# Kernel tuning notes

Measured on AMD Instinct MI355X. Metric: run time of the kernel, lower is better.

The kernel has to match this reference:

```python
import jax, jax.numpy as jnp
import numpy as np

MAX_SENT_LEN = 28
B, LAT, D, E = 2048, 256, 1024, 256
LN_EPS = 1e-5


def setup_inputs() -> dict:
    key = jax.random.key(0)
    ks = jax.random.split(key, 10)
    s = 0.05
    return {
        "z": jax.random.normal(ks[0], (B, LAT), jnp.float32),
        "true_inp": jax.random.normal(ks[1], (B, MAX_SENT_LEN, E), jnp.float32),
        "tf_mask": jax.random.bernoulli(ks[2], 0.5, (MAX_SENT_LEN,)),
        "fc_w": jax.random.normal(ks[3], (D, LAT), jnp.float32) * s,
        "fc_b": jnp.zeros((D,), jnp.float32),
        "ln_w": jnp.ones((D,), jnp.float32),
        "ln_b": jnp.zeros((D,), jnp.float32),
        "w_ih": jax.random.normal(ks[4], (3 * D, D), jnp.float32) * s,
        "b_ih": jnp.zeros((3 * D,), jnp.float32),
        "w_hh": jax.random.normal(ks[5], (3 * D, D), jnp.float32) * s,
        "b_hh": jnp.zeros((3 * D,), jnp.float32),
    }


def reference(z, true_inp, tf_mask, fc_w, fc_b, ln_w, ln_b, w_ih, b_ih, w_hh, b_hh):
    # fc + layer norm -> initial hidden and (repeated) step input, [B, D]
    x = z @ fc_w.T + fc_b
    mu = jnp.mean(x, axis=-1, keepdims=True)
    var = jnp.mean(jnp.square(x - mu), axis=-1, keepdims=True)
    x = (x - mu) * jax.lax.rsqrt(var + LN_EPS) * ln_w + ln_b

    # encoded input is identical at every step -> precompute input gates once
    gi = x @ w_ih.T + b_ih                      # [B, 3D]
    i_r, i_z, i_n = jnp.split(gi, 3, axis=-1)

    # true_inp.repeat(1,1,repeating).transpose(1,0) -> [T, B, D]
    rep = D // E
    true_rep = jnp.transpose(jnp.tile(true_inp, (1, 1, rep)), (1, 0, 2))

    def step(h, inputs):
        t_inp, m = inputs
        h_in = jnp.where(m, t_inp, h)           # teacher-forcing branch
        gh = h_in @ w_hh.T + b_hh               # [B, 3D]
        h_r, h_z, h_n = jnp.split(gh, 3, axis=-1)
        r = jax.nn.sigmoid(i_r + h_r)
        u = jax.nn.sigmoid(i_z + h_z)
        n = jnp.tanh(i_n + r * h_n)
        h_new = (1.0 - u) * n + u * h_in
        return h_new, h_new

    _, outs = jax.lax.scan(step, x, (true_rep, tf_mask))
    return outs                                  # [T, B, D]
```

## Files before the change

### kernel.cpp

```cpp
#include <hip/hip_runtime.h>
#include <hip/hip_bf16.h>

#define TSTEPS 28

typedef __attribute__((ext_vector_type(8))) short bf16x8;
typedef __attribute__((ext_vector_type(4))) float f32x4;
typedef __attribute__((ext_vector_type(4))) unsigned short u16x4;
typedef __hip_bfloat16 bf16;

__device__ __forceinline__ unsigned short f2b(float f) {
  bf16 h = __float2bfloat16(f);
  return *reinterpret_cast<unsigned short*>(&h);
}
__device__ __forceinline__ float b2f(unsigned short u) {
  bf16 h = *reinterpret_cast<bf16*>(&u);
  return __bfloat162float(h);
}

__device__ __forceinline__ void gload16(const void* g, void* l) {
  __builtin_amdgcn_global_load_lds(
      (const __attribute__((address_space(1))) void*)g,
      (__attribute__((address_space(3))) void*)l, 16, 0, 0);
}

__device__ __forceinline__ float sigm(float x) { return 1.f / (1.f + __expf(-x)); }
__device__ __forceinline__ float tanh_fast(float x) {
  const float e2 = __expf(2.f * x);
  return 1.f - 2.f / (e2 + 1.f);
}

__device__ __forceinline__ bf16x8 cvt8(const float* src) {
  const float4 v0 = *(const float4*)src;
  const float4 v1 = *(const float4*)(src + 4);
  bf16x8 sv;
  sv[0] = (short)f2b(v0.x); sv[1] = (short)f2b(v0.y);
  sv[2] = (short)f2b(v0.z); sv[3] = (short)f2b(v0.w);
  sv[4] = (short)f2b(v1.x); sv[5] = (short)f2b(v1.y);
  sv[6] = (short)f2b(v1.z); sv[7] = (short)f2b(v1.w);
  return sv;
}

__global__ void conv_kernel(const float* __restrict__ in, unsigned short* __restrict__ out, int n4) {
  int i = blockIdx.x * blockDim.x + threadIdx.x;
  const int stride = gridDim.x * blockDim.x;
  for (; i < n4; i += stride) {
    const float4 v = *(const float4*)&in[(size_t)i * 4];
    u16x4 o;
    o.x = f2b(v.x); o.y = f2b(v.y); o.z = f2b(v.z); o.w = f2b(v.w);
    *(u16x4*)&out[(size_t)i * 4] = o;
  }
}

__global__ __launch_bounds__(256) void convw_kernel(const float* __restrict__ whh,
                                                    unsigned short* __restrict__ whhb,
                                                    unsigned short* __restrict__ whf) {
  const int idx = blockIdx.x * 256 + threadIdx.x;
  const int n = idx >> 6, k4 = (idx & 63) << 2;
  const float* r = &whh[(size_t)n * 1024 + k4];
  const float4 a = *(const float4*)r;
  const float4 b = *(const float4*)(r + 256);
  const float4 c = *(const float4*)(r + 512);
  const float4 d = *(const float4*)(r + 768);
  u16x4 oa, ob, oc, od, of;
  oa.x = f2b(a.x); oa.y = f2b(a.y); oa.z = f2b(a.z); oa.w = f2b(a.w);
  ob.x = f2b(b.x); ob.y = f2b(b.y); ob.z = f2b(b.z); ob.w = f2b(b.w);
  oc.x = f2b(c.x); oc.y = f2b(c.y); oc.z = f2b(c.z); oc.w = f2b(c.w);
  od.x = f2b(d.x); od.y = f2b(d.y); od.z = f2b(d.z); od.w = f2b(d.w);
  of.x = f2b(a.x + b.x + c.x + d.x);
  of.y = f2b(a.y + b.y + c.y + d.y);
  of.z = f2b(a.z + b.z + c.z + d.z);
  of.w = f2b(a.w + b.w + c.w + d.w);
  unsigned short* wb = &whhb[(size_t)n * 1024 + k4];
  *(u16x4*)(wb)       = oa;
  *(u16x4*)(wb + 256) = ob;
  *(u16x4*)(wb + 512) = oc;
  *(u16x4*)(wb + 768) = od;
  *(u16x4*)&whf[(size_t)n * 256 + k4] = of;
}

__global__ __launch_bounds__(256, 2) void gemm_fc_kernel(
    const float* __restrict__ A, const float* __restrict__ W,
    const float* __restrict__ bias, float* __restrict__ out) {
  constexpr int K = 256, NT = K / 32;
  __shared__ __align__(16) bf16 lds[2][6144];
  const int tid = threadIdx.x;
  const int lane = tid & 63;
  const int l15 = lane & 15, l4 = lane >> 4;
  const int wid = tid >> 6, wm = wid >> 1, wn = wid & 1;
  const int m0 = blockIdx.x * 128, n0 = blockIdx.y * 64;
  const int ra = tid >> 2, cb = (tid & 3) * 8;

  f32x4 acc[4][2] = {};

  auto STAGE = [&](int buf, int kt) {
    const int k0 = kt * 32;
    *(bf16x8*)&lds[buf][tid * 8]        = cvt8(&A[(size_t)(m0 + ra) * K + k0 + cb]);
    *(bf16x8*)&lds[buf][2048 + tid * 8] = cvt8(&A[(size_t)(m0 + 64 + ra) * K + k0 + cb]);
    *(bf16x8*)&lds[buf][4096 + tid * 8] = cvt8(&W[(size_t)(n0 + ra) * K + k0 + cb]);
  };

  STAGE(0, 0);
  __syncthreads();
  for (int kt = 0; kt < NT; ++kt) {
    const int buf = kt & 1;
    if (kt + 1 < NT) STAGE(buf ^ 1, kt + 1);
    bf16x8 af[4], bfr[2];
#pragma unroll
    for (int m = 0; m < 4; ++m)
      af[m] = *(const bf16x8*)&lds[buf][(wm * 64 + m * 16 + l15) * 32 + l4 * 8];
#pragma unroll
    for (int n = 0; n < 2; ++n)
      bfr[n] = *(const bf16x8*)&lds[buf][4096 + (wn * 32 + n * 16 + l15) * 32 + l4 * 8];
#pragma unroll
    for (int m = 0; m < 4; ++m)
#pragma unroll
      for (int n = 0; n < 2; ++n)
        acc[m][n] = __builtin_amdgcn_mfma_f32_16x16x32_bf16(af[m], bfr[n], acc[m][n], 0, 0, 0);
    __syncthreads();
  }

#pragma unroll
  for (int m = 0; m < 4; ++m) {
#pragma unroll
    for (int n = 0; n < 2; ++n) {
      const int col = n0 + wn * 32 + n * 16 + l15;
      const int rowb = m0 + wm * 64 + m * 16 + l4 * 4;
      const float bv = bias[col];
#pragma unroll
      for (int r = 0; r < 4; ++r)
        out[(size_t)(rowb + r) * 1024 + col] = acc[m][n][r] + bv;
    }
  }
}

__global__ __launch_bounds__(256) void ln_kernel(const float* __restrict__ x,
                                                 const float* __restrict__ w,
                                                 const float* __restrict__ b,
                                                 bf16* __restrict__ h0b,
                                                 float* __restrict__ h0f) {
  const int row = blockIdx.x, tid = threadIdx.x;
  const float4 v = *(const float4*)&x[(size_t)row * 1024 + tid * 4];
  float vv[4] = {v.x, v.y, v.z, v.w};
  float s = vv[0] + vv[1] + vv[2] + vv[3];
  float sq = vv[0] * vv[0] + vv[1] * vv[1] + vv[2] * vv[2] + vv[3] * vv[3];
#pragma unroll
  for (int off = 32; off; off >>= 1) {
    s += __shfl_down(s, off);
    sq += __shfl_down(sq, off);
  }
  __shared__ float sa[4], sb[4];
  const int lane = tid & 63, wid = tid >> 6;
  if (lane == 0) { sa[wid] = s; sb[wid] = sq; }
  __syncthreads();
  s = sa[0] + sa[1] + sa[2] + sa[3];
  sq = sb[0] + sb[1] + sb[2] + sb[3];
  const float mu = s * (1.f / 1024.f);
  const float var = sq * (1.f / 1024.f) - mu * mu;
  const float rs = rsqrtf(var + 1e-5f);
#pragma unroll
  for (int j = 0; j < 4; ++j) {
    const int c = tid * 4 + j;
    const float xv = (vv[j] - mu) * rs * w[c] + b[c];
    h0b[(size_t)row * 1024 + c] = __float2bfloat16(xv);
    h0f[(size_t)row * 1024 + c] = xv;
  }
}

__global__ __launch_bounds__(512, 4) void gemm_gi_kernel(
    const bf16* __restrict__ A,
    const float* __restrict__ W,
    const float* __restrict__ bias,
    unsigned short* __restrict__ out) {
  __shared__ __align__(16) bf16 lds[2][16384];
  const int tid = threadIdx.x;
  const int lane = tid & 63, l15 = lane & 15, l4 = lane >> 4;
  const int wid = tid >> 6, wm = wid >> 2, wn = wid & 3;
  const int n0 = blockIdx.x * 64, m0 = blockIdx.y * 64;

  f32x4 acc[3][2] = {};

  auto STAGE = [&](int buf, int kt) {
    const int k0 = kt * 64;
    {
      const int c = tid;
      const int row = c >> 3, kk = ((c & 7) ^ (row & 7)) * 8;
      gload16(&A[(size_t)(m0 + row) * 1024 + k0 + kk], &lds[buf][c * 8]);
    }
#pragma unroll
    for (int j = 0; j < 3; ++j) {
      const int c = tid + j * 512;
      const int row = c >> 3, kk = ((c & 7) ^ (row & 7)) * 8;
      *(bf16x8*)&lds[buf][4096 + c * 8] =
          cvt8(&W[(size_t)((row >> 6) * 1024 + n0 + (row & 63)) * 1024 + k0 + kk]);
    }
  };

  STAGE(0, 0);
  __syncthreads();
  for (int kt = 0; kt < 16; ++kt) {
    const int buf = kt & 1;
    if (kt + 1 < 16) STAGE(buf ^ 1, kt + 1);
#pragma unroll
    for (int ks = 0; ks < 2; ++ks) {
      const int x = (((ks << 2) | l4) ^ (l15 & 7)) * 8;
      bf16x8 af[2], bfr[3];
#pragma unroll
      for (int m = 0; m < 2; ++m)
        af[m] = *(const bf16x8*)&lds[buf][(wm * 32 + m * 16 + l15) * 64 + x];
#pragma unroll
      for (int g = 0; g < 3; ++g)
        bfr[g] = *(const bf16x8*)&lds[buf][4096 + (g * 64 + wn * 16 + l15) * 64 + x];
#pragma unroll
      for (int g = 0; g < 3; ++g)
#pragma unroll
        for (int m = 0; m < 2; ++m)
          acc[g][m] = __builtin_amdgcn_mfma_f32_16x16x32_bf16(af[m], bfr[g], acc[g][m], 0, 0, 0);
    }
    __syncthreads();
  }

  const int col = n0 + wn * 16 + l15;
#pragma unroll
  for (int g = 0; g < 3; ++g) {
    const float bv = bias[g * 1024 + col];
#pragma unroll
    for (int m = 0; m < 2; ++m) {
      const int rowb = m0 + wm * 32 + m * 16 + l4 * 4;
#pragma unroll
      for (int r = 0; r < 4; ++r)
        out[(size_t)(rowb + r) * 3072 + g * 1024 + col] = f2b(acc[g][m][r] + bv);
    }
  }
}

__global__ __launch_bounds__(512, 2) void batch_pair_kernel(
    const bf16* __restrict__ trueb,
    const int* __restrict__ tfmask,
    const bf16* __restrict__ whf,
    const float* __restrict__ bhh,
    const unsigned short* __restrict__ gib,
    float* __restrict__ out) {
  const int p = blockIdx.z;
  const int t1 = 2 * p, t2 = 2 * p + 1;
  const bool m1 = tfmask[t1] != 0;
  const bool m2 = tfmask[t2] != 0;
  if (!m1 && !m2) return;
  __shared__ __align__(16) bf16 lds[2][20480];
  const int tid = threadIdx.x;
  const int lane = tid & 63, l15 = lane & 15, l4 = lane >> 4;
  const int wid = tid >> 6, wm = wid >> 2, wn = wid & 3;
  const int n0 = blockIdx.x * 64, m0 = blockIdx.y * 64;

  f32x4 acc1[3][2] = {}, acc2[3][2] = {};

  auto STAGE = [&](int buf, int kt) {
    const int k0 = kt * 64;
    {
      const int c = tid;
      const int row = c >> 3, kk = ((c & 7) ^ (row & 7)) * 8;
      if (m1)
        gload16(&trueb[((size_t)(m0 + row) * TSTEPS + t1) * 256 + k0 + kk], &lds[buf][c * 8]);
      if (m2)
        gload16(&trueb[((size_t)(m0 + row) * TSTEPS + t2) * 256 + k0 + kk],
                &lds[buf][4096 + c * 8]);
    }
#pragma unroll
    for (int j = 0; j < 3; ++j) {
      const int c = tid + j * 512;
      const int row = c >> 3, kk = ((c & 7) ^ (row & 7)) * 8;
      gload16(&whf[(size_t)((row >> 6) * 1024 + n0 + (row & 63)) * 256 + k0 + kk],
              &lds[buf][8192 + c * 8]);
    }
  };

  STAGE(0, 0);
  __syncthreads();
  for (int kt = 0; kt < 4; ++kt) {
    const int buf = kt & 1;
    if (kt + 1 < 4) STAGE(buf ^ 1, kt + 1);
#pragma unroll
    for (int ks = 0; ks < 2; ++ks) {
      const int x = (((ks << 2) | l4) ^ (l15 & 7)) * 8;
      bf16x8 bfr[3];
#pragma unroll
      for (int g = 0; g < 3; ++g)
        bfr[g] = *(const bf16x8*)&lds[buf][8192 + (g * 64 + wn * 16 + l15) * 64 + x];
      if (m1) {
        bf16x8 af[2];
#pragma unroll
        for (int m = 0; m < 2; ++m)
          af[m] = *(const bf16x8*)&lds[buf][(wm * 32 + m * 16 + l15) * 64 + x];
#pragma unroll
        for (int g = 0; g < 3; ++g)
#pragma unroll
          for (int m = 0; m < 2; ++m)
            acc1[g][m] = __builtin_amdgcn_mfma_f32_16x16x32_bf16(af[m], bfr[g], acc1[g][m], 0, 0, 0);
      }
      if (m2) {
        bf16x8 af[2];
#pragma unroll
        for (int m = 0; m < 2; ++m)
          af[m] = *(const bf16x8*)&lds[buf][4096 + (wm * 32 + m * 16 + l15) * 64 + x];
#pragma unroll
        for (int g = 0; g < 3; ++g)
#pragma unroll
          for (int m = 0; m < 2; ++m)
            acc2[g][m] = __builtin_amdgcn_mfma_f32_16x16x32_bf16(af[m], bfr[g], acc2[g][m], 0, 0, 0);
      }
    }
    __syncthreads();
  }

  const int col = n0 + wn * 16 + l15;
  const float br = bhh[col], bz = bhh[col + 1024], bn_ = bhh[col + 2048];
  const unsigned short* tb = (const unsigned short*)trueb;

  auto EPI = [&](int t, f32x4 (&acc)[3][2]) {
    float* outT = out + (size_t)t * 2048 * 1024;
#pragma unroll
    for (int m = 0; m < 2; ++m) {
      const int rowb = m0 + wm * 32 + m * 16 + l4 * 4;
#pragma unroll
      for (int r = 0; r < 4; ++r) {
        const int row = rowb + r;
        const unsigned short* girow = &gib[(size_t)row * 3072];
        const float ir = b2f(girow[col]), iz = b2f(girow[col + 1024]), inn = b2f(girow[col + 2048]);
        const float hr = acc[0][m][r] + br;
        const float hz = acc[1][m][r] + bz;
        const float hn = acc[2][m][r] + bn_;
        const float hinv = b2f(tb[((size_t)row * TSTEPS + t) * 256 + (col & 255)]);
        const float rg = sigm(ir + hr);
        const float ug = sigm(iz + hz);
        const float ng = tanh_fast(inn + rg * hn);
        outT[(size_t)row * 1024 + col] = (1.f - ug) * ng + ug * hinv;
      }
    }
  };
  if (m1) EPI(t1, acc1);
  if (m2) EPI(t2, acc2);
}

__global__ __launch_bounds__(512, 4) void step_kernel(
    const float* __restrict__ prevf,
    const bf16* __restrict__ hbfprev,
    bf16* __restrict__ hbfout,
    const int* __restrict__ tfmask,
    const bf16* __restrict__ whh,
    const float* __restrict__ bhh,
    const unsigned short* __restrict__ gib,
    float* __restrict__ out, int t) {
  if (tfmask[t] != 0) return;
  const bool predf32 = (t == 0) || (tfmask[t - 1] != 0);
  const int lid = blockIdx.x;
  const int xcd = lid & 7, rest = lid >> 3;
  const int m0 = (rest & 31) * 64;
  const int n0 = ((xcd << 1) | (rest >> 5)) * 64;

  __shared__ __align__(16) bf16 lds[2][16384];
  const int tid = threadIdx.x;
  const int lane = tid & 63, l15 = lane & 15, l4 = lane >> 4;
  const int wid = tid >> 6, wm = wid >> 2, wn = wid & 3;

  f32x4 acc[3][2] = {};

  auto STAGE = [&](int buf, int kt) {
    const int k0 = kt * 64;
    {
      const int c = tid;
      const int row = c >> 3, kk = ((c & 7) ^ (row & 7)) * 8;
      if (predf32) {
        *(bf16x8*)&lds[buf][c * 8] = cvt8(&prevf[(size_t)(m0 + row) * 1024 + k0 + kk]);
      } else {
        gload16(&hbfprev[(size_t)(m0 + row) * 1024 + k0 + kk], &lds[buf][c * 8]);
      }
    }
#pragma unroll
    for (int j = 0; j < 3; ++j) {
      const int c = tid + j * 512;
      const int row = c >> 3, kk = ((c & 7) ^ (row & 7)) * 8;
      gload16(&whh[(size_t)((row >> 6) * 1024 + n0 + (row & 63)) * 1024 + k0 + kk],
              &lds[buf][4096 + c * 8]);
    }
  };

  STAGE(0, 0);
  __syncthreads();
  for (int kt = 0; kt < 16; ++kt) {
    const int buf = kt & 1;
    if (kt + 1 < 16) STAGE(buf ^ 1, kt + 1);
#pragma unroll
    for (int ks = 0; ks < 2; ++ks) {
      const int x = (((ks << 2) | l4) ^ (l15 & 7)) * 8;
      bf16x8 af[2], bfr[3];
#pragma unroll
      for (int m = 0; m < 2; ++m)
        af[m] = *(const bf16x8*)&lds[buf][(wm * 32 + m * 16 + l15) * 64 + x];
#pragma unroll
      for (int g = 0; g < 3; ++g)
        bfr[g] = *(const bf16x8*)&lds[buf][4096 + (g * 64 + wn * 16 + l15) * 64 + x];
#pragma unroll
      for (int g = 0; g < 3; ++g)
#pragma unroll
        for (int m = 0; m < 2; ++m)
          acc[g][m] = __builtin_amdgcn_mfma_f32_16x16x32_bf16(af[m], bfr[g], acc[g][m], 0, 0, 0);
    }
    __syncthreads();
  }

  float* outT = out + (size_t)t * 2048 * 1024;
  const int col = n0 + wn * 16 + l15;
  const float br = bhh[col], bz = bhh[col + 1024], bn_ = bhh[col + 2048];
#pragma unroll
  for (int m = 0; m < 2; ++m) {
    const int rowb = m0 + wm * 32 + m * 16 + l4 * 4;
#pragma unroll
    for (int r = 0; r < 4; ++r) {
      const int row = rowb + r;
      const unsigned short* girow = &gib[(size_t)row * 3072];
      const float ir = b2f(girow[col]), iz = b2f(girow[col + 1024]), inn = b2f(girow[col + 2048]);
      const float hr = acc[0][m][r] + br;
      const float hz = acc[1][m][r] + bz;
      const float hn = acc[2][m][r] + bn_;
      const float hinv = prevf[(size_t)row * 1024 + col];
      const float rg = sigm(ir + hr);
      const float ug = sigm(iz + hz);
      const float ng = tanh_fast(inn + rg * hn);
      const float hnew = (1.f - ug) * ng + ug * hinv;
      outT[(size_t)row * 1024 + col] = hnew;
      hbfout[(size_t)row * 1024 + col] = __float2bfloat16(hnew);
    }
  }
}

extern "C" void kernel_launch(void* const* d_in, const int* in_sizes, int n_in,
                              void* d_out, int out_size, void* d_ws, size_t ws_size,
                              hipStream_t stream) {
  (void)in_sizes; (void)n_in; (void)out_size; (void)ws_size;
  const float* z = (const float*)d_in[0];
  const float* trueinp = (const float*)d_in[1];
  const int* tfmask = (const int*)d_in[2];
  const float* fc_w = (const float*)d_in[3];
  const float* fc_b = (const float*)d_in[4];
  const float* ln_w = (const float*)d_in[5];
  const float* ln_b = (const float*)d_in[6];
  const float* w_ih = (const float*)d_in[7];
  const float* b_ih = (const float*)d_in[8];
  const float* w_hh = (const float*)d_in[9];
  const float* b_hh = (const float*)d_in[10];
  float* out = (float*)d_out;

  char* ws = (char*)d_ws;
  size_t o = 0;
  float* xraw = (float*)(ws + o); o += (size_t)2048 * 1024 * 4;
  float* h0f  = (float*)(ws + o); o += (size_t)2048 * 1024 * 4;
  unsigned short* gib = (unsigned short*)(ws + o); o += (size_t)2048 * 3072 * 2;
  bf16* h0b   = (bf16*)(ws + o);  o += (size_t)2048 * 1024 * 2;
  bf16* hbf0  = (bf16*)(ws + o);  o += (size_t)2048 * 1024 * 2;
  bf16* hbf1  = (bf16*)(ws + o);  o += (size_t)2048 * 1024 * 2;
  bf16* whhb  = (bf16*)(ws + o);  o += (size_t)3072 * 1024 * 2;
  bf16* whf   = (bf16*)(ws + o);  o += (size_t)3072 * 256 * 2;
  bf16* trueb = (bf16*)(ws + o);  o += (size_t)2048 * TSTEPS * 256 * 2;

  convw_kernel<<<768, 256, 0, stream>>>(w_hh, (unsigned short*)whhb, (unsigned short*)whf);
  conv_kernel<<<2048, 256, 0, stream>>>(trueinp, (unsigned short*)trueb, 2048 * TSTEPS * 256 / 4);

  gemm_fc_kernel<<<dim3(16, 16), 256, 0, stream>>>(z, fc_w, fc_b, xraw);
  ln_kernel<<<2048, 256, 0, stream>>>(xraw, ln_w, ln_b, h0b, h0f);
  gemm_gi_kernel<<<dim3(16, 32), 512, 0, stream>>>(h0b, w_ih, b_ih, gib);

  batch_pair_kernel<<<dim3(16, 32, TSTEPS / 2), 512, 0, stream>>>(trueb, tfmask, whf,
                                                                  b_hh, gib, out);

  const float* prev = h0f;
  for (int t = 0; t < TSTEPS; ++t) {
    bf16* hw = (t & 1) ? hbf1 : hbf0;
    const bf16* hr = (t & 1) ? hbf0 : hbf1;
    step_kernel<<<512, 512, 0, stream>>>(prev, hr, hw, tfmask, whhb, b_hh, gib, out, t);
    prev = out + (size_t)t * 2048 * 1024;
  }
}
```

Measured before the change: 512.4 us.

## Batch first-level recurrent steps after teacher-forced steps into one launch

Non-teacher-forced steps whose previous step was teacher-forced (or t=0) only depend on outputs the batch_pair kernel already produced. They are now computed together in one 2D-grid kernel (level1b) across all timesteps instead of serially. The per-step loop starts at t=1 and skips those steps, so fewer step launches do real work. An unused level1_kernel variant is also added, which only adds code.

```diff
diff --git a/kernel.cpp b/kernel.cpp
--- a/kernel.cpp
+++ b/kernel.cpp
@@ -340,6 +340,196 @@
   if (m2) EPI(t2, acc2);
 }
 
+__global__ __launch_bounds__(512, 4) void level1_kernel(
+    const bf16* __restrict__ h0b,
+    const int* __restrict__ tfmask,
+    const bf16* __restrict__ whh,
+    const float* __restrict__ bhh,
+    const unsigned short* __restrict__ gib,
+    float* __restrict__ out) {
+  const int t = blockIdx.y;
+  if (tfmask[t] != 0) return;
+  if (t > 0 && tfmask[t - 1] == 0) return;
+  const float* prevf = (t == 0) ? nullptr : out + (size_t)(t - 1) * 2048 * 1024;
+
+  const int lid = blockIdx.x;
+  const int xcd = lid & 7, rest = lid >> 3;
+  const int m0 = (rest & 31) * 64;
+  const int n0 = ((xcd << 1) | (rest >> 5)) * 64;
+
+  __shared__ __align__(16) bf16 lds[2][16384];
+  const int tid = threadIdx.x;
+  const int lane = tid & 63, l15 = lane & 15, l4 = lane >> 4;
+  const int wid = tid >> 6, wm = wid >> 2, wn = wid & 3;
+
+  f32x4 acc[3][2] = {};
+
+  auto STAGE = [&](int buf, int kt) {
+    const int k0 = kt * 64;
+    {
+      const int c = tid;
+      const int row = c >> 3, kk = ((c & 7) ^ (row & 7)) * 8;
+      if (t == 0) {
+        gload16(&h0b[(size_t)(m0 + row) * 1024 + k0 + kk], &lds[buf][c * 8]);
+      } else {
+        *(bf16x8*)&lds[buf][c * 8] = cvt8(&prevf[(size_t)(m0 + row) * 1024 + k0 + kk]);
+      }
+    }
+#pragma unroll
+    for (int j = 0; j < 3; ++j) {
+      const int c = tid + j * 512;
+      const int row = c >> 3, kk = ((c & 7) ^ (row & 7)) * 8;
+      gload16(&whh[(size_t)((row >> 6) * 1024 + n0 + (row & 63)) * 1024 + k0 + kk],
+              &lds[buf][4096 + c * 8]);
+    }
+  };
+
+  STAGE(0, 0);
+  __syncthreads();
+  for (int kt = 0; kt < 16; ++kt) {
+    const int buf = kt & 1;
+    if (kt + 1 < 16) STAGE(buf ^ 1, kt + 1);
+#pragma unroll
+    for (int ks = 0; ks < 2; ++ks) {
+      const int x = (((ks << 2) | l4) ^ (l15 & 7)) * 8;
+      bf16x8 af[2], bfr[3];
+#pragma unroll
+      for (int m = 0; m < 2; ++m)
+        af[m] = *(const bf16x8*)&lds[buf][(wm * 32 + m * 16 + l15) * 64 + x];
+#pragma unroll
+      for (int g = 0; g < 3; ++g)
+        bfr[g] = *(const bf16x8*)&lds[buf][4096 + (g * 64 + wn * 16 + l15) * 64 + x];
+#pragma unroll
+      for (int g = 0; g < 3; ++g)
+#pragma unroll
+        for (int m = 0; m < 2; ++m)
+          acc[g][m] = __builtin_amdgcn_mfma_f32_16x16x32_bf16(af[m], bfr[g], acc[g][m], 0, 0, 0);
+    }
+    __syncthreads();
+  }
+
+  float* outT = out + (size_t)t * 2048 * 1024;
+  const int col = n0 + wn * 16 + l15;
+  const float br = bhh[col], bz = bhh[col + 1024], bn_ = bhh[col + 2048];
+#pragma unroll
+  for (int m = 0; m < 2; ++m) {
+    const int rowb = m0 + wm * 32 + m * 16 + l4 * 4;
+#pragma unroll
+    for (int r = 0; r < 4; ++r) {
+      const int row = rowb + r;
+      const unsigned short* girow = &gib[(size_t)row * 3072];
+      const float ir = b2f(girow[col]), iz = b2f(girow[col + 1024]), inn = b2f(girow[col + 2048]);
+      const float hr = acc[0][m][r] + br;
+      const float hz = acc[1][m][r] + bz;
+      const float hn = acc[2][m][r] + bn_;
+      float hinv;
+      if (t == 0) {
+        hinv = 0.f;
+      } else {
+        hinv = prevf[(size_t)row * 1024 + col];
+      }
+      const float rg = sigm(ir + hr);
+      const float ug = sigm(iz + hz);
+      const float ng = tanh_fast(inn + rg * hn);
+      const float hnew = (1.f - ug) * ng + ug * hinv;
+      outT[(size_t)row * 1024 + col] = hnew;
+    }
+  }
+}
+
+__global__ __launch_bounds__(512, 4) void level1b_kernel(
+    const bf16* __restrict__ h0b,
+    const float* __restrict__ h0f,
+    const int* __restrict__ tfmask,
+    const bf16* __restrict__ whh,
+    const float* __restrict__ bhh,
+    const unsigned short* __restrict__ gib,
+    float* __restrict__ out) {
+  const int t = blockIdx.y;
+  if (tfmask[t] != 0) return;
+  if (t > 0 && tfmask[t - 1] == 0) return;
+  const float* prevf = (t == 0) ? h0f : out + (size_t)(t - 1) * 2048 * 1024;
+  const bool abf = (t == 0);
+
+  const int lid = blockIdx.x;
+  const int xcd = lid & 7, rest = lid >> 3;
+  const int m0 = (rest & 31) * 64;
+  const int n0 = ((xcd << 1) | (rest >> 5)) * 64;
+
+  __shared__ __align__(16) bf16 lds[2][16384];
+  const int tid = threadIdx.x;
+  const int lane = tid & 63, l15 = lane & 15, l4 = lane >> 4;
+  const int wid = tid >> 6, wm = wid >> 2, wn = wid & 3;
+
+  f32x4 acc[3][2] = {};
+
+  auto STAGE = [&](int buf, int kt) {
+    const int k0 = kt * 64;
+    {
+      const int c = tid;
+      const int row = c >> 3, kk = ((c & 7) ^ (row & 7)) * 8;
+      if (abf) {
+        gload16(&h0b[(size_t)(m0 + row) * 1024 + k0 + kk], &lds[buf][c * 8]);
+      } else {
+        *(bf16x8*)&lds[buf][c * 8] = cvt8(&prevf[(size_t)(m0 + row) * 1024 + k0 + kk]);
+      }
+    }
+#pragma unroll
+    for (int j = 0; j < 3; ++j) {
+      const int c = tid + j * 512;
+      const int row = c >> 3, kk = ((c & 7) ^ (row & 7)) * 8;
+      gload16(&whh[(size_t)((row >> 6) * 1024 + n0 + (row & 63)) * 1024 + k0 + kk],
+              &lds[buf][4096 + c * 8]);
+    }
+  };
+
+  STAGE(0, 0);
+  __syncthreads();
+  for (int kt = 0; kt < 16; ++kt) {
+    const int buf = kt & 1;
+    if (kt + 1 < 16) STAGE(buf ^ 1, kt + 1);
+#pragma unroll
+    for (int ks = 0; ks < 2; ++ks) {
+      const int x = (((ks << 2) | l4) ^ (l15 & 7)) * 8;
+      bf16x8 af[2], bfr[3];
+#pragma unroll
+      for (int m = 0; m < 2; ++m)
+        af[m] = *(const bf16x8*)&lds[buf][(wm * 32 + m * 16 + l15) * 64 + x];
+#pragma unroll
+      for (int g = 0; g < 3; ++g)
+        bfr[g] = *(const bf16x8*)&lds[buf][4096 + (g * 64 + wn * 16 + l15) * 64 + x];
+#pragma unroll
+      for (int g = 0; g < 3; ++g)
+#pragma unroll
+        for (int m = 0; m < 2; ++m)
+          acc[g][m] = __builtin_amdgcn_mfma_f32_16x16x32_bf16(af[m], bfr[g], acc[g][m], 0, 0, 0);
+    }
+    __syncthreads();
+  }
+
+  float* outT = out + (size_t)t * 2048 * 1024;
+  const int col = n0 + wn * 16 + l15;
+  const float br = bhh[col], bz = bhh[col + 1024], bn_ = bhh[col + 2048];
+#pragma unroll
+  for (int m = 0; m < 2; ++m) {
+    const int rowb = m0 + wm * 32 + m * 16 + l4 * 4;
+#pragma unroll
+    for (int r = 0; r < 4; ++r) {
+      const int row = rowb + r;
+      const unsigned short* girow = &gib[(size_t)row * 3072];
+      const float ir = b2f(girow[col]), iz = b2f(girow[col + 1024]), inn = b2f(girow[col + 2048]);
+      const float hr = acc[0][m][r] + br;
+      const float hz = acc[1][m][r] + bz;
+      const float hn = acc[2][m][r] + bn_;
+      const float hinv = prevf[(size_t)row * 1024 + col];
+      const float rg = sigm(ir + hr);
+      const float ug = sigm(iz + hz);
+      const float ng = tanh_fast(inn + rg * hn);
+      outT[(size_t)row * 1024 + col] = (1.f - ug) * ng + ug * hinv;
+    }
+  }
+}
+
 __global__ __launch_bounds__(512, 4) void step_kernel(
     const float* __restrict__ prevf,
     const bf16* __restrict__ hbfprev,
@@ -350,7 +540,8 @@
     const unsigned short* __restrict__ gib,
     float* __restrict__ out, int t) {
   if (tfmask[t] != 0) return;
-  const bool predf32 = (t == 0) || (tfmask[t - 1] != 0);
+  if (tfmask[t - 1] != 0) return;
+  const bool predf32 = (t == 1) || (tfmask[t - 2] != 0);
   const int lid = blockIdx.x;
   const int xcd = lid & 7, rest = lid >> 3;
   const int m0 = (rest & 31) * 64;
@@ -471,11 +662,13 @@
   batch_pair_kernel<<<dim3(16, 32, TSTEPS / 2), 512, 0, stream>>>(trueb, tfmask, whf,
                                                                   b_hh, gib, out);
 
-  const float* prev = h0f;
-  for (int t = 0; t < TSTEPS; ++t) {
+  level1b_kernel<<<dim3(512, TSTEPS), 512, 0, stream>>>(h0b, h0f, tfmask, whhb, b_hh,
+                                                        gib, out);
+
+  for (int t = 1; t < TSTEPS; ++t) {
     bf16* hw = (t & 1) ? hbf1 : hbf0;
     const bf16* hr = (t & 1) ? hbf0 : hbf1;
+    const float* prev = out + (size_t)(t - 1) * 2048 * 1024;
     step_kernel<<<512, 512, 0, stream>>>(prev, hr, hw, tfmask, whhb, b_hh, gib, out, t);
-    prev = out + (size_t)t * 2048 * 1024;
-  }
-}
+  }
+}
```

After: 510.2 us. About the same (-0.4%).

## Batch first non-teacher-forced GRU steps across timesteps into one launch

Applied to the files above, without the earlier changes.

Adds a level-1 kernel that computes, in a single grid over all timesteps, every non-teacher-forced step whose predecessor is teacher-forced or is the initial state. These steps do not depend on each other, so they no longer need one serial launch each. The per-step loop now handles only steps that follow another computed step. To feed the batched kernel bf16 operands, the teacher-forced batch kernel also writes a bf16 copy of its outputs into a large workspace buffer. That buffer is used only if the workspace is big enough, and it adds extra global writes.

```diff
diff --git a/kernel.cpp b/kernel.cpp
--- a/kernel.cpp
+++ b/kernel.cpp
@@ -239,7 +239,8 @@
     const bf16* __restrict__ whf,
     const float* __restrict__ bhh,
     const unsigned short* __restrict__ gib,
-    float* __restrict__ out) {
+    float* __restrict__ out,
+    bf16* __restrict__ hbt) {
   const int p = blockIdx.z;
   const int t1 = 2 * p, t2 = 2 * p + 1;
   const bool m1 = tfmask[t1] != 0;
@@ -317,6 +318,7 @@
 
   auto EPI = [&](int t, f32x4 (&acc)[3][2]) {
     float* outT = out + (size_t)t * 2048 * 1024;
+    bf16* hbtT = hbt ? hbt + (size_t)t * 2048 * 1024 : nullptr;
 #pragma unroll
     for (int m = 0; m < 2; ++m) {
       const int rowb = m0 + wm * 32 + m * 16 + l4 * 4;
@@ -332,12 +334,108 @@
         const float rg = sigm(ir + hr);
         const float ug = sigm(iz + hz);
         const float ng = tanh_fast(inn + rg * hn);
-        outT[(size_t)row * 1024 + col] = (1.f - ug) * ng + ug * hinv;
+        const float hnew = (1.f - ug) * ng + ug * hinv;
+        outT[(size_t)row * 1024 + col] = hnew;
+        if (hbtT) hbtT[(size_t)row * 1024 + col] = __float2bfloat16(hnew);
       }
     }
   };
   if (m1) EPI(t1, acc1);
   if (m2) EPI(t2, acc2);
+}
+
+__global__ __launch_bounds__(512, 4) void level1b_kernel(
+    const bf16* __restrict__ h0b,
+    const float* __restrict__ h0f,
+    const bf16* __restrict__ hbt,
+    const int* __restrict__ tfmask,
+    const bf16* __restrict__ whh,
+    const float* __restrict__ bhh,
+    const unsigned short* __restrict__ gib,
+    float* __restrict__ out) {
+  const int t = blockIdx.y;
+  if (tfmask[t] != 0) return;
+  if (t > 0 && tfmask[t - 1] == 0) return;
+  const float* prevf = (t == 0) ? h0f : out + (size_t)(t - 1) * 2048 * 1024;
+  const bf16* prevb = (t == 0) ? h0b : (hbt ? hbt + (size_t)(t - 1) * 2048 * 1024 : nullptr);
+
+  const int lid = blockIdx.x;
+  const int xcd = lid & 7, rest = lid >> 3;
+  const int m0 = (rest & 31) * 64;
+  const int n0 = ((xcd << 1) | (rest >> 5)) * 64;
+
+  __shared__ __align__(16) bf16 lds[2][16384];
+  const int tid = threadIdx.x;
+  const int lane = tid & 63, l15 = lane & 15, l4 = lane >> 4;
+  const int wid = tid >> 6, wm = wid >> 2, wn = wid & 3;
+
+  f32x4 acc[3][2] = {};
+
+  auto STAGE = [&](int buf, int kt) {
+    const int k0 = kt * 64;
+    {
+      const int c = tid;
+      const int row = c >> 3, kk = ((c & 7) ^ (row & 7)) * 8;
+      if (prevb) {
+        gload16(&prevb[(size_t)(m0 + row) * 1024 + k0 + kk], &lds[buf][c * 8]);
+      } else {
+        *(bf16x8*)&lds[buf][c * 8] = cvt8(&prevf[(size_t)(m0 + row) * 1024 + k0 + kk]);
+      }
+    }
+#pragma unroll
+    for (int j = 0; j < 3; ++j) {
+      const int c = tid + j * 512;
+      const int row = c >> 3, kk = ((c & 7) ^ (row & 7)) * 8;
+      gload16(&whh[(size_t)((row >> 6) * 1024 + n0 + (row & 63)) * 1024 + k0 + kk],
+              &lds[buf][4096 + c * 8]);
+    }
+  };
+
+  STAGE(0, 0);
+  __syncthreads();
+  for (int kt = 0; kt < 16; ++kt) {
+    const int buf = kt & 1;
+    if (kt + 1 < 16) STAGE(buf ^ 1, kt + 1);
+#pragma unroll
+    for (int ks = 0; ks < 2; ++ks) {
+      const int x = (((ks << 2) | l4) ^ (l15 & 7)) * 8;
+      bf16x8 af[2], bfr[3];
+#pragma unroll
+      for (int m = 0; m < 2; ++m)
+        af[m] = *(const bf16x8*)&lds[buf][(wm * 32 + m * 16 + l15) * 64 + x];
+#pragma unroll
+      for (int g = 0; g < 3; ++g)
+        bfr[g] = *(const bf16x8*)&lds[buf][4096 + (g * 64 + wn * 16 + l15) * 64 + x];
+#pragma unroll
+      for (int g = 0; g < 3; ++g)
+#pragma unroll
+        for (int m = 0; m < 2; ++m)
+          acc[g][m] = __builtin_amdgcn_mfma_f32_16x16x32_bf16(af[m], bfr[g], acc[g][m], 0, 0, 0);
+    }
+    __syncthreads();
+  }
+
+  float* outT = out + (size_t)t * 2048 * 1024;
+  const int col = n0 + wn * 16 + l15;
+  const float br = bhh[col], bz = bhh[col + 1024], bn_ = bhh[col + 2048];
+#pragma unroll
+  for (int m = 0; m < 2; ++m) {
+    const int rowb = m0 + wm * 32 + m * 16 + l4 * 4;
+#pragma unroll
+    for (int r = 0; r < 4; ++r) {
+      const int row = rowb + r;
+      const unsigned short* girow = &gib[(size_t)row * 3072];
+      const float ir = b2f(girow[col]), iz = b2f(girow[col + 1024]), inn = b2f(girow[col + 2048]);
+      const float hr = acc[0][m][r] + br;
+      const float hz = acc[1][m][r] + bz;
+      const float hn = acc[2][m][r] + bn_;
+      const float hinv = prevf[(size_t)row * 1024 + col];
+      const float rg = sigm(ir + hr);
+      const float ug = sigm(iz + hz);
+      const float ng = tanh_fast(inn + rg * hn);
+      outT[(size_t)row * 1024 + col] = (1.f - ug) * ng + ug * hinv;
+    }
+  }
 }
 
 __global__ __launch_bounds__(512, 4) void step_kernel(
@@ -350,7 +448,8 @@
     const unsigned short* __restrict__ gib,
     float* __restrict__ out, int t) {
   if (tfmask[t] != 0) return;
-  const bool predf32 = (t == 0) || (tfmask[t - 1] != 0);
+  if (tfmask[t - 1] != 0) return;
+  const bool predf32 = (t == 1) || (tfmask[t - 2] != 0);
   const int lid = blockIdx.x;
   const int xcd = lid & 7, rest = lid >> 3;
   const int m0 = (rest & 31) * 64;
@@ -435,7 +534,7 @@
 extern "C" void kernel_launch(void* const* d_in, const int* in_sizes, int n_in,
                               void* d_out, int out_size, void* d_ws, size_t ws_size,
                               hipStream_t stream) {
-  (void)in_sizes; (void)n_in; (void)out_size; (void)ws_size;
+  (void)in_sizes; (void)n_in; (void)out_size;
   const float* z = (const float*)d_in[0];
   const float* trueinp = (const float*)d_in[1];
   const int* tfmask = (const int*)d_in[2];
@@ -460,6 +559,10 @@
   bf16* whhb  = (bf16*)(ws + o);  o += (size_t)3072 * 1024 * 2;
   bf16* whf   = (bf16*)(ws + o);  o += (size_t)3072 * 256 * 2;
   bf16* trueb = (bf16*)(ws + o);  o += (size_t)2048 * TSTEPS * 256 * 2;
+  bf16* hbt   = (bf16*)(ws + o);
+  const size_t need_hbt = o + (size_t)TSTEPS * 2048 * 1024 * 2;
+  const bool use_hbt = (ws_size >= need_hbt);
+  bf16* hbt_arg = use_hbt ? hbt : nullptr;
 
   convw_kernel<<<768, 256, 0, stream>>>(w_hh, (unsigned short*)whhb, (unsigned short*)whf);
   conv_kernel<<<2048, 256, 0, stream>>>(trueinp, (unsigned short*)trueb, 2048 * TSTEPS * 256 / 4);
@@ -469,13 +572,15 @@
   gemm_gi_kernel<<<dim3(16, 32), 512, 0, stream>>>(h0b, w_ih, b_ih, gib);
 
   batch_pair_kernel<<<dim3(16, 32, TSTEPS / 2), 512, 0, stream>>>(trueb, tfmask, whf,
-                                                                  b_hh, gib, out);
-
-  const float* prev = h0f;
-  for (int t = 0; t < TSTEPS; ++t) {
+                                                                  b_hh, gib, out, hbt_arg);
+
+  level1b_kernel<<<dim3(512, TSTEPS), 512, 0, stream>>>(h0b, h0f, hbt_arg, tfmask, whhb,
+                                                        b_hh, gib, out);
+
+  for (int t = 1; t < TSTEPS; ++t) {
     bf16* hw = (t & 1) ? hbf1 : hbf0;
     const bf16* hr = (t & 1) ? hbf0 : hbf1;
+    const float* prev = out + (size_t)(t - 1) * 2048 * 1024;
     step_kernel<<<512, 512, 0, stream>>>(prev, hr, hw, tfmask, whhb, b_hh, gib, out, t);
-    prev = out + (size_t)t * 2048 * 1024;
-  }
-}
+  }
+}
```

New measurement: 501.5 us, median of 2. 2.1% less time.
